# Optimization experiments

Hardware: AMD Instinct MI355X
Metric: run time of the kernel (lower is better)

## Reference

```python
import jax, jax.numpy as jnp
import numpy as np

B, N, C = 4, 4096, 384
NH, SR = 6, 2
HD = C // NH
LN_EPS = 1e-5


def setup_inputs() -> dict:
    key = jax.random.key(0)
    ks = jax.random.split(key, 8)
    s = 0.02
    return {
        "x": jax.random.normal(ks[0], (B, N, C), dtype=jnp.float32),
        "Wq": jax.random.normal(ks[1], (C, C), dtype=jnp.float32) * s,
        "bq": jnp.zeros((C,), jnp.float32),
        "Wk": jax.random.normal(ks[2], (C, C), dtype=jnp.float32) * s,
        "bk": jnp.zeros((C,), jnp.float32),
        "Wv": jax.random.normal(ks[3], (C, C), dtype=jnp.float32) * s,
        "bv": jnp.zeros((C,), jnp.float32),
        "sr_w": jax.random.normal(ks[4], (C, 1, SR, SR), dtype=jnp.float32) * s,  # depthwise OIHW
        "sr_b": jnp.zeros((C,), jnp.float32),
        "ln_g": jnp.ones((C,), jnp.float32),
        "ln_b": jnp.zeros((C,), jnp.float32),
        "Wp": jax.random.normal(ks[5], (C, C), dtype=jnp.float32) * s,
        "bp": jnp.zeros((C,), jnp.float32),
        "H": 64,
        "W": 64,
    }


def reference(x, Wq, bq, Wk, bk, Wv, bv, sr_w, sr_b, ln_g, ln_b, Wp, bp, H, W):
    Bv, Nv, Cv = x.shape
    scale = HD ** (-0.5)

    def heads(t):  # (B, L, C) -> (B, NH, L, HD)
        return t.reshape(Bv, -1, NH, HD).transpose(0, 2, 1, 3)

    q = heads(x @ Wq.T + bq)

    # spatial reduction: depthwise strided conv on (B, C, H, W)
    x_ = x.transpose(0, 2, 1).reshape(Bv, Cv, H, W)
    x_ = jax.lax.conv_general_dilated(
        x_, sr_w, window_strides=(SR, SR), padding="VALID",
        dimension_numbers=("NCHW", "OIHW", "NCHW"), feature_group_count=Cv,
    ) + sr_b[None, :, None, None]
    x_ = x_.reshape(Bv, Cv, -1).transpose(0, 2, 1)  # (B, Nk, C)

    # LayerNorm over channels
    mu = jnp.mean(x_, axis=-1, keepdims=True)
    var = jnp.mean((x_ - mu) ** 2, axis=-1, keepdims=True)
    x_ = (x_ - mu) / jnp.sqrt(var + LN_EPS) * ln_g + ln_b

    k = heads(x_ @ Wk.T + bk)
    v = heads(x_ @ Wv.T + bv)

    attn = jnp.einsum("bhqd,bhkd->bhqk", q, k) * scale
    attn = jnp.sign(attn) * jax.nn.softmax(jnp.abs(attn), axis=-1)  # 'neg' softmax
    out = jnp.einsum("bhqk,bhkd->bhqd", attn, v)
    out = out.transpose(0, 2, 1, 3).reshape(Bv, Nv, Cv)
    return out @ Wp.T + bp
```

## Files before the change

kernel.cpp:

```cpp
#include <hip/hip_runtime.h>
#include <hip/hip_bf16.h>
#include <math.h>

#define BB 4
#define NN 4096
#define CC 384
#define NHH 6
#define HDD 64
#define NKK 1024
#define LN_EPS 1e-5f

typedef _Float16 half8 __attribute__((ext_vector_type(8)));
typedef _Float16 half4v __attribute__((ext_vector_type(4)));
typedef _Float16 half2v __attribute__((ext_vector_type(2)));
typedef float f32x4 __attribute__((ext_vector_type(4)));

#define MFMA16(a, b, c) __builtin_amdgcn_mfma_f32_16x16x32_f16((a), (b), (c), 0, 0, 0)

#define GLL16(src, dst)                                                       \
    __builtin_amdgcn_global_load_lds(                                         \
        (const __attribute__((address_space(1))) void*)(src),                 \
        (__attribute__((address_space(3))) void*)(dst), 16, 0, 0)

template<int AIN, int WIN, int OUT>
__global__ __launch_bounds__(256) void gemm_mf(
    const void* __restrict__ A0, const void* __restrict__ A1,
    const _Float16* __restrict__ Whi, const _Float16* __restrict__ Wlo,
    const float* __restrict__ bias, _Float16* __restrict__ Yhi,
    _Float16* __restrict__ Ylo, float* __restrict__ Yf, float scale)
{
    constexpr bool SPLIT = (AIN != 2);
    __shared__ _Float16 AhiS[128 * 64];
    __shared__ _Float16 AloS[SPLIT ? 128 * 64 : 64];
    __shared__ _Float16 WhiS[64 * 64];
    __shared__ _Float16 WloS[(WIN == 1) ? 64 * 64 : 64];

    const int tid = threadIdx.x;
    const int bm = blockIdx.x * 128;
    const int bn = blockIdx.y * 64;
    const int w = tid >> 6, lane = tid & 63;
    const int g = lane >> 4, n15 = lane & 15;

    f32x4 zero4 = {0.f, 0.f, 0.f, 0.f};
    f32x4 acc_hi[2][4], acc_lo[SPLIT ? 2 : 1][SPLIT ? 4 : 1];
#pragma unroll
    for (int mf = 0; mf < 2; ++mf)
#pragma unroll
        for (int nt = 0; nt < 4; ++nt) {
            acc_hi[mf][nt] = zero4;
            if (SPLIT) acc_lo[mf][nt] = zero4;
        }

    for (int k0 = 0; k0 < CC; k0 += 64) {
        __syncthreads();
        if (AIN == 0) {
            const float* A = (const float*)A0;
#pragma unroll
            for (int i = 0; i < 8; ++i) {
                int id = tid + 256 * i;
                int row = id >> 4, c4 = (id & 15) * 4;
                float4 av = *reinterpret_cast<const float4*>(A + (size_t)(bm + row) * CC + k0 + c4);
                int el = row * 64 + (((c4 >> 3) ^ (row & 7)) * 8) + (c4 & 7);
                float vv[4] = {av.x, av.y, av.z, av.w};
                half4v hi, lo;
#pragma unroll
                for (int e = 0; e < 4; ++e) {
                    _Float16 h = (_Float16)vv[e];
                    hi[e] = h;
                    lo[e] = (_Float16)((vv[e] - (float)h) * 256.0f);
                }
                *reinterpret_cast<half4v*>(&AhiS[el]) = hi;
                *reinterpret_cast<half4v*>(&AloS[el]) = lo;
            }
        } else {
            const _Float16* A = (const _Float16*)A0;
#pragma unroll
            for (int i = 0; i < 4; ++i) {
                int id = tid + 256 * i;
                int row = id >> 3, dg = id & 7;
                half8 av = *reinterpret_cast<const half8*>(A + (size_t)(bm + row) * CC + k0 + dg * 8);
                int el = row * 64 + ((dg ^ (row & 7)) * 8);
                *reinterpret_cast<half8*>(&AhiS[el]) = av;
            }
        }
#pragma unroll
        for (int i = 0; i < 2; ++i) {
            int id = tid + 256 * i;
            int row = id >> 3, dg = id & 7;
            size_t go = (size_t)(bn + row) * CC + k0 + dg * 8;
            half8 wh = *reinterpret_cast<const half8*>(Whi + go);
            int el = row * 64 + ((dg ^ (row & 7)) * 8);
            *reinterpret_cast<half8*>(&WhiS[el]) = wh;
            if (WIN == 1) {
                half8 wl = *reinterpret_cast<const half8*>(Wlo + go);
                *reinterpret_cast<half8*>(&WloS[el]) = wl;
            }
        }
        __syncthreads();
#pragma unroll
        for (int kc = 0; kc < 2; ++kc) {
            const int blk = kc * 4 + g;
            half8 a_hi[2], a_lo[2], b_hi[4], b_lo[4];
#pragma unroll
            for (int mf = 0; mf < 2; ++mf) {
                int row = w * 32 + mf * 16 + n15;
                int el = row * 64 + ((blk ^ (row & 7)) * 8);
                a_hi[mf] = *reinterpret_cast<const half8*>(&AhiS[el]);
                if (SPLIT) a_lo[mf] = *reinterpret_cast<const half8*>(&AloS[el]);
            }
#pragma unroll
            for (int nt = 0; nt < 4; ++nt) {
                int row = nt * 16 + n15;
                int el = row * 64 + ((blk ^ (row & 7)) * 8);
                b_hi[nt] = *reinterpret_cast<const half8*>(&WhiS[el]);
                if (WIN == 1) b_lo[nt] = *reinterpret_cast<const half8*>(&WloS[el]);
            }
#pragma unroll
            for (int mf = 0; mf < 2; ++mf)
#pragma unroll
                for (int nt = 0; nt < 4; ++nt) {
                    acc_hi[mf][nt] = MFMA16(a_hi[mf], b_hi[nt], acc_hi[mf][nt]);
                    if (SPLIT) {
                        acc_lo[mf][nt] = MFMA16(a_hi[mf], b_lo[nt], acc_lo[mf][nt]);
                        acc_lo[mf][nt] = MFMA16(a_lo[mf], b_hi[nt], acc_lo[mf][nt]);
                    }
                }
        }
    }
#pragma unroll
    for (int nt = 0; nt < 4; ++nt) {
        int col = bn + nt * 16 + n15;
        float bc = bias[col];
#pragma unroll
        for (int mf = 0; mf < 2; ++mf)
#pragma unroll
            for (int r = 0; r < 4; ++r) {
                size_t row = bm + w * 32 + mf * 16 + g * 4 + r;
                float y = acc_hi[mf][nt][r];
                if (SPLIT) y += acc_lo[mf][nt][r] * (1.0f / 256.0f);
                y = (y + bc) * scale;
                if (OUT == 0) {
                    _Float16 h = (_Float16)y;
                    Yhi[row * CC + col] = h;
                    Ylo[row * CC + col] = (_Float16)((y - (float)h) * 256.0f);
                } else {
                    Yf[row * CC + col] = y;
                }
            }
    }
}

__global__ __launch_bounds__(256) void gemm_kv(
    const _Float16* __restrict__ Ah, const _Float16* __restrict__ Al,
    const _Float16* __restrict__ Wkh, const _Float16* __restrict__ Wkl,
    const _Float16* __restrict__ Wvh, const _Float16* __restrict__ Wvl,
    const float* __restrict__ bk, const float* __restrict__ bv,
    _Float16* __restrict__ Khi, _Float16* __restrict__ Klo,
    _Float16* __restrict__ Vt)
{
    __shared__ _Float16 AhiS[128 * 64];
    __shared__ _Float16 AloS[128 * 64];
    __shared__ _Float16 WhiS[64 * 64];
    __shared__ _Float16 WloS[64 * 64];

    const int tid = threadIdx.x;
    const int bm = blockIdx.x * 128;
    const int bn = blockIdx.y * 64;
    const int isV = blockIdx.z;
    const _Float16* Whi = isV ? Wvh : Wkh;
    const _Float16* Wlo = isV ? Wvl : Wkl;
    const float* bias = isV ? bv : bk;
    const int w = tid >> 6, lane = tid & 63;
    const int g = lane >> 4, n15 = lane & 15;

    f32x4 zero4 = {0.f, 0.f, 0.f, 0.f};
    f32x4 acc_hi[2][4], acc_lo[2][4];
#pragma unroll
    for (int mf = 0; mf < 2; ++mf)
#pragma unroll
        for (int nt = 0; nt < 4; ++nt) { acc_hi[mf][nt] = zero4; acc_lo[mf][nt] = zero4; }

    for (int k0 = 0; k0 < CC; k0 += 64) {
        __syncthreads();
#pragma unroll
        for (int i = 0; i < 4; ++i) {
            int id = tid + 256 * i;
            int row = id >> 3, dg = id & 7;
            size_t go = (size_t)(bm + row) * CC + k0 + dg * 8;
            half8 hv = *reinterpret_cast<const half8*>(Ah + go);
            half8 lv = *reinterpret_cast<const half8*>(Al + go);
            int el = row * 64 + ((dg ^ (row & 7)) * 8);
            *reinterpret_cast<half8*>(&AhiS[el]) = hv;
            *reinterpret_cast<half8*>(&AloS[el]) = lv;
        }
#pragma unroll
        for (int i = 0; i < 2; ++i) {
            int id = tid + 256 * i;
            int row = id >> 3, dg = id & 7;
            size_t go = (size_t)(bn + row) * CC + k0 + dg * 8;
            half8 wh = *reinterpret_cast<const half8*>(Whi + go);
            half8 wl = *reinterpret_cast<const half8*>(Wlo + go);
            int el = row * 64 + ((dg ^ (row & 7)) * 8);
            *reinterpret_cast<half8*>(&WhiS[el]) = wh;
            *reinterpret_cast<half8*>(&WloS[el]) = wl;
        }
        __syncthreads();
#pragma unroll
        for (int kc = 0; kc < 2; ++kc) {
            const int blk = kc * 4 + g;
            half8 a_hi[2], a_lo[2], b_hi[4], b_lo[4];
#pragma unroll
            for (int mf = 0; mf < 2; ++mf) {
                int row = w * 32 + mf * 16 + n15;
                int el = row * 64 + ((blk ^ (row & 7)) * 8);
                a_hi[mf] = *reinterpret_cast<const half8*>(&AhiS[el]);
                a_lo[mf] = *reinterpret_cast<const half8*>(&AloS[el]);
            }
#pragma unroll
            for (int nt = 0; nt < 4; ++nt) {
                int row = nt * 16 + n15;
                int el = row * 64 + ((blk ^ (row & 7)) * 8);
                b_hi[nt] = *reinterpret_cast<const half8*>(&WhiS[el]);
                b_lo[nt] = *reinterpret_cast<const half8*>(&WloS[el]);
            }
#pragma unroll
            for (int mf = 0; mf < 2; ++mf)
#pragma unroll
                for (int nt = 0; nt < 4; ++nt) {
                    acc_hi[mf][nt] = MFMA16(a_hi[mf], b_hi[nt], acc_hi[mf][nt]);
                    acc_lo[mf][nt] = MFMA16(a_hi[mf], b_lo[nt], acc_lo[mf][nt]);
                    acc_lo[mf][nt] = MFMA16(a_lo[mf], b_hi[nt], acc_lo[mf][nt]);
                }
        }
    }
#pragma unroll
    for (int nt = 0; nt < 4; ++nt) {
        int col = bn + nt * 16 + n15;
        float bc = bias[col];
#pragma unroll
        for (int mf = 0; mf < 2; ++mf)
#pragma unroll
            for (int r = 0; r < 4; ++r) {
                size_t row = bm + w * 32 + mf * 16 + g * 4 + r;
                float y = acc_hi[mf][nt][r] + acc_lo[mf][nt][r] * (1.0f / 256.0f) + bc;
                if (!isV) {
                    _Float16 h = (_Float16)y;
                    Khi[row * CC + col] = h;
                    Klo[row * CC + col] = (_Float16)((y - (float)h) * 256.0f);
                } else {
                    Vt[((row >> 10) * CC + col) * NKK + (row & 1023)] = (_Float16)y;
                }
            }
    }
}

__global__ __launch_bounds__(128)
void srconv_splitw(const float* __restrict__ x, const float* __restrict__ srw,
                   const float* __restrict__ srb, const float* __restrict__ g,
                   const float* __restrict__ beta,
                   _Float16* __restrict__ xrh, _Float16* __restrict__ xrl,
                   const float* __restrict__ Wq, const float* __restrict__ Wk,
                   const float* __restrict__ Wv, const float* __restrict__ Wp,
                   _Float16* __restrict__ wqh, _Float16* __restrict__ wql,
                   _Float16* __restrict__ wkh, _Float16* __restrict__ wkl,
                   _Float16* __restrict__ wvh, _Float16* __restrict__ wvl,
                   _Float16* __restrict__ wph) {
    const int bid = blockIdx.x;
    const int tid = threadIdx.x;
    if (bid >= BB * NKK) {
        int i = (bid - BB * NKK) * 128 + tid;
        float q = Wq[i], k = Wk[i], v = Wv[i], p = Wp[i];
        _Float16 h;
        h = (_Float16)q; wqh[i] = h; wql[i] = (_Float16)((q - (float)h) * 256.0f);
        h = (_Float16)k; wkh[i] = h; wkl[i] = (_Float16)((k - (float)h) * 256.0f);
        h = (_Float16)v; wvh[i] = h; wvl[i] = (_Float16)((v - (float)h) * 256.0f);
        wph[i] = (_Float16)p;
        return;
    }
    const int row = bid;
    const int b  = row >> 10;
    const int nk = row & 1023;
    const int oy = nk >> 5;
    const int ox = nk & 31;
    const int n0 = (2 * oy) * 64 + 2 * ox;
    const float* xb = x + ((size_t)b * NN + n0) * CC;

    float vals[3];
    float lsum = 0.f, lsum2 = 0.f;
#pragma unroll
    for (int i = 0; i < 3; ++i) {
        const int c = tid + i * 128;
        const float4 w = *reinterpret_cast<const float4*>(srw + (size_t)c * 4);
        float v = xb[c] * w.x + xb[CC + c] * w.y +
                  xb[(size_t)64 * CC + c] * w.z + xb[(size_t)65 * CC + c] * w.w + srb[c];
        vals[i] = v;
        lsum += v;
        lsum2 += v * v;
    }
#pragma unroll
    for (int off = 32; off; off >>= 1) {
        lsum  += __shfl_down(lsum, off);
        lsum2 += __shfl_down(lsum2, off);
    }
    __shared__ float ssum[2], ssum2[2];
    if ((tid & 63) == 0) { ssum[tid >> 6] = lsum; ssum2[tid >> 6] = lsum2; }
    __syncthreads();
    const float tot  = ssum[0] + ssum[1];
    const float tot2 = ssum2[0] + ssum2[1];
    const float mu  = tot * (1.0f / 384.0f);
    const float var = tot2 * (1.0f / 384.0f) - mu * mu;
    const float rstd = 1.0f / sqrtf(var + LN_EPS);

    _Float16* oh = xrh + (size_t)row * CC;
    _Float16* ol = xrl + (size_t)row * CC;
#pragma unroll
    for (int i = 0; i < 3; ++i) {
        const int c = tid + i * 128;
        float v = (vals[i] - mu) * rstd * g[c] + beta[c];
        _Float16 h = (_Float16)v;
        oh[c] = h;
        ol[c] = (_Float16)((v - (float)h) * 256.0f);
    }
}

__global__ __launch_bounds__(256, 3)
void attn_mfma(const _Float16* __restrict__ Qhi, const _Float16* __restrict__ Qlo,
               const _Float16* __restrict__ Khi, const _Float16* __restrict__ Klo,
               const _Float16* __restrict__ Vt, _Float16* __restrict__ O)
{
    __shared__ _Float16 KhiS[2][32 * 64];
    __shared__ _Float16 KloS[2][32 * 64];
    __shared__ _Float16 VTS[2][64 * 32];
    __shared__ _Float16 PWS[4][1024];

    const int tid = threadIdx.x;
    const int w = tid >> 6, lane = tid & 63;
    const int g = lane >> 4, q15 = lane & 15;
    _Float16* PW = PWS[w];

    const int qt = blockIdx.x, h = blockIdx.y, b = blockIdx.z;

    half8 qh[2][2], ql[2][2];
    {
        size_t qoff = ((size_t)b * NN + qt * 128 + w * 32 + q15) * CC + h * 64 + g * 8;
#pragma unroll
        for (int f = 0; f < 2; ++f) {
            qh[f][0] = *reinterpret_cast<const half8*>(Qhi + qoff + f * 16 * CC);
            qh[f][1] = *reinterpret_cast<const half8*>(Qhi + qoff + f * 16 * CC + 32);
            ql[f][0] = *reinterpret_cast<const half8*>(Qlo + qoff + f * 16 * CC);
            ql[f][1] = *reinterpret_cast<const half8*>(Qlo + qoff + f * 16 * CC + 32);
        }
    }
    asm volatile("s_waitcnt vmcnt(0)" ::: "memory");

    const int krow = tid >> 3, kdg = tid & 7;
    const int kscol = (kdg ^ (krow & 7)) * 8;
    const _Float16* ksrc = Khi + ((size_t)b * NKK + krow) * CC + h * 64 + kscol;
    const _Float16* lsrc = Klo + ((size_t)b * NKK + krow) * CC + h * 64 + kscol;
    const int vd = tid >> 2, vkb = tid & 3;
    const _Float16* vsrc = Vt + ((size_t)b * CC + h * 64 + vd) * NKK + ((vkb ^ ((vd >> 1) & 3)) * 8);

    f32x4 zero4 = {0.f, 0.f, 0.f, 0.f};
    f32x4 o[2][4];
#pragma unroll
    for (int f = 0; f < 2; ++f)
#pragma unroll
        for (int nt = 0; nt < 4; ++nt) o[f][nt] = zero4;
    float l[2] = {0.f, 0.f};

#define ISSUE(kt, buf)                                                        \
    {                                                                         \
        GLL16(ksrc + (size_t)(kt) * 32 * CC, &KhiS[buf][tid * 8]);            \
        GLL16(lsrc + (size_t)(kt) * 32 * CC, &KloS[buf][tid * 8]);            \
        GLL16(vsrc + (kt) * 32,              &VTS[buf][tid * 8]);             \
    }

    auto COMPUTE = [&](const _Float16* KH, const _Float16* KL, const _Float16* VT) {
        float ls[2] = {0.f, 0.f};
#pragma unroll
        for (int mt = 0; mt < 2; ++mt) {
            f32x4 sh[2], sl[2];
#pragma unroll
            for (int f = 0; f < 2; ++f) { sh[f] = zero4; sl[f] = zero4; }
            __builtin_amdgcn_s_setprio(1);
#pragma unroll
            for (int kc = 0; kc < 2; ++kc) {
                int key = mt * 16 + q15;
                int el = key * 64 + (((kc * 4 + g) ^ (key & 7)) * 8);
                half8 ah = *reinterpret_cast<const half8*>(&KH[el]);
                half8 al = *reinterpret_cast<const half8*>(&KL[el]);
#pragma unroll
                for (int f = 0; f < 2; ++f) {
                    sh[f] = MFMA16(ah, qh[f][kc], sh[f]);
                    sl[f] = MFMA16(ah, ql[f][kc], sl[f]);
                    sl[f] = MFMA16(al, qh[f][kc], sl[f]);
                }
            }
            __builtin_amdgcn_s_setprio(0);
            int elw = q15 * 32 + (((mt * 2 + (g >> 1)) ^ ((q15 >> 1) & 3)) * 8) + (g & 1) * 4;
#pragma unroll
            for (int f = 0; f < 2; ++f) {
                half4v pk;
#pragma unroll
                for (int r = 0; r < 4; ++r) {
                    float sv = sh[f][r] + sl[f][r] * (1.0f / 256.0f);
                    float e = __expf(fabsf(sv));
                    ls[f] += e;
                    pk[r] = (_Float16)__builtin_copysignf(e, sv);
                }
                *reinterpret_cast<half4v*>(&PW[elw + f * 512]) = pk;
            }
        }
#pragma unroll
        for (int f = 0; f < 2; ++f) {
            ls[f] += __shfl_xor(ls[f], 16);
            ls[f] += __shfl_xor(ls[f], 32);
            l[f] += ls[f];
        }

        __builtin_amdgcn_s_setprio(1);
        {
            int pel = q15 * 32 + ((g ^ ((q15 >> 1) & 3)) * 8);
            half8 pa0 = *reinterpret_cast<const half8*>(&PW[pel]);
            half8 pa1 = *reinterpret_cast<const half8*>(&PW[pel + 512]);
#pragma unroll
            for (int nt = 0; nt < 4; ++nt) {
                int d = nt * 16 + q15;
                int vel = d * 32 + ((g ^ ((d >> 1) & 3)) * 8);
                half8 vb = *reinterpret_cast<const half8*>(&VT[vel]);
                o[0][nt] = MFMA16(pa0, vb, o[0][nt]);
                o[1][nt] = MFMA16(pa1, vb, o[1][nt]);
            }
        }
        __builtin_amdgcn_s_setprio(0);
    };

    ISSUE(0, 0);

#pragma unroll 1
    for (int kt2 = 0; kt2 < 32; kt2 += 2) {
        ISSUE(kt2 + 1, 1);
        asm volatile("s_waitcnt vmcnt(3)" ::: "memory");
        __builtin_amdgcn_s_barrier();
        COMPUTE(KhiS[0], KloS[0], VTS[0]);
        asm volatile("" ::: "memory");
        __builtin_amdgcn_s_barrier();

        if (kt2 + 2 < 32) {
            ISSUE(kt2 + 2, 0);
            asm volatile("s_waitcnt vmcnt(3)" ::: "memory");
        } else {
            asm volatile("s_waitcnt vmcnt(0)" ::: "memory");
        }
        __builtin_amdgcn_s_barrier();
        COMPUTE(KhiS[1], KloS[1], VTS[1]);
        asm volatile("" ::: "memory");
        __builtin_amdgcn_s_barrier();
    }
#undef ISSUE

#pragma unroll
    for (int f = 0; f < 2; ++f) {
        float rl = 1.0f / l[f];
        float rlq[4];
#pragma unroll
        for (int r = 0; r < 4; ++r) rlq[r] = __shfl(rl, g * 4 + r);
#pragma unroll
        for (int nt = 0; nt < 4; ++nt)
#pragma unroll
            for (int r = 0; r < 4; ++r) {
                size_t row = (size_t)b * NN + qt * 128 + w * 32 + f * 16 + g * 4 + r;
                O[row * CC + h * 64 + nt * 16 + q15] = (_Float16)(o[f][nt][r] * rlq[r]);
            }
    }
}

extern "C" void kernel_launch(void* const* d_in, const int* in_sizes, int n_in,
                              void* d_out, int out_size, void* d_ws, size_t ws_size,
                              hipStream_t stream) {
    const float* x   = (const float*)d_in[0];
    const float* Wq  = (const float*)d_in[1];
    const float* bq  = (const float*)d_in[2];
    const float* Wk  = (const float*)d_in[3];
    const float* bk  = (const float*)d_in[4];
    const float* Wv  = (const float*)d_in[5];
    const float* bv  = (const float*)d_in[6];
    const float* srw = (const float*)d_in[7];
    const float* srb = (const float*)d_in[8];
    const float* lng = (const float*)d_in[9];
    const float* lnb = (const float*)d_in[10];
    const float* Wp  = (const float*)d_in[11];
    const float* bp  = (const float*)d_in[12];
    float* out = (float*)d_out;

    char* wsb = (char*)d_ws;
    _Float16* Qhi  = (_Float16*)wsb;
    _Float16* Qlo  = (_Float16*)(wsb + 12582912);
    _Float16* XRhi = (_Float16*)(wsb + 25165824);
    _Float16* XRlo = (_Float16*)(wsb + 28311552);
    _Float16* Khi  = (_Float16*)(wsb + 31457280);
    _Float16* Klo  = (_Float16*)(wsb + 34603008);
    _Float16* Vt   = (_Float16*)(wsb + 37748736);
    _Float16* Wqh  = (_Float16*)(wsb + 40894464);
    _Float16* Wql  = Wqh + 147456;
    _Float16* Wkh  = Wql + 147456;
    _Float16* Wkl  = Wkh + 147456;
    _Float16* Wvh  = Wkl + 147456;
    _Float16* Wvl  = Wvh + 147456;
    _Float16* Wph  = Wvl + 147456;
    _Float16* Ob   = Qlo;

    srconv_splitw<<<dim3(BB * NKK + 1152), dim3(128), 0, stream>>>(
        x, srw, srb, lng, lnb, XRhi, XRlo,
        Wq, Wk, Wv, Wp, Wqh, Wql, Wkh, Wkl, Wvh, Wvl, Wph);
    gemm_mf<0, 1, 0><<<dim3(128, 6), 256, 0, stream>>>(
        x, nullptr, Wqh, Wql, bq, Qhi, Qlo, nullptr, 0.125f);
    gemm_kv<<<dim3(32, 6, 2), 256, 0, stream>>>(
        XRhi, XRlo, Wkh, Wkl, Wvh, Wvl, bk, bv, Khi, Klo, Vt);
    attn_mfma<<<dim3(32, 6, 4), 256, 0, stream>>>(Qhi, Qlo, Khi, Klo, Vt, Ob);
    gemm_mf<2, 2, 2><<<dim3(128, 6), 256, 0, stream>>>(
        Ob, nullptr, Wph, nullptr, bp, nullptr, nullptr, out, 1.0f);
}
```

Before: 129.4 us.

## Merge Q/K/V projections into one launch and triple-buffer attention K/V tiles

Merges the Q projection and the K/V projection kernels into a single kernel whose blocks choose their mode from the block index, cutting one launch and letting the small K/V work fill gaps left by the Q work. The attention kernel moves from double to triple buffering of K/V tiles, so each prefetch is issued right after a compute step instead of behind a second barrier. The cross-lane row-sum reduction is also deferred to the end of the attention kernel. The output GEMM is split into its own specialised kernel. Triple buffering uses more LDS per block, which may reduce occupancy.

```diff
diff --git a/kernel.cpp b/kernel.cpp
--- a/kernel.cpp
+++ b/kernel.cpp
@@ -22,18 +22,12 @@
         (const __attribute__((address_space(1))) void*)(src),                 \
         (__attribute__((address_space(3))) void*)(dst), 16, 0, 0)
 
-template<int AIN, int WIN, int OUT>
-__global__ __launch_bounds__(256) void gemm_mf(
-    const void* __restrict__ A0, const void* __restrict__ A1,
-    const _Float16* __restrict__ Whi, const _Float16* __restrict__ Wlo,
-    const float* __restrict__ bias, _Float16* __restrict__ Yhi,
-    _Float16* __restrict__ Ylo, float* __restrict__ Yf, float scale)
+__global__ __launch_bounds__(256) void gemm_out(
+    const _Float16* __restrict__ A, const _Float16* __restrict__ Whi,
+    const float* __restrict__ bias, float* __restrict__ Yf)
 {
-    constexpr bool SPLIT = (AIN != 2);
     __shared__ _Float16 AhiS[128 * 64];
-    __shared__ _Float16 AloS[SPLIT ? 128 * 64 : 64];
     __shared__ _Float16 WhiS[64 * 64];
-    __shared__ _Float16 WloS[(WIN == 1) ? 64 * 64 : 64];
 
     const int tid = threadIdx.x;
     const int bm = blockIdx.x * 128;
@@ -42,24 +36,116 @@
     const int g = lane >> 4, n15 = lane & 15;
 
     f32x4 zero4 = {0.f, 0.f, 0.f, 0.f};
-    f32x4 acc_hi[2][4], acc_lo[SPLIT ? 2 : 1][SPLIT ? 4 : 1];
+    f32x4 acc[2][4];
 #pragma unroll
     for (int mf = 0; mf < 2; ++mf)
 #pragma unroll
-        for (int nt = 0; nt < 4; ++nt) {
-            acc_hi[mf][nt] = zero4;
-            if (SPLIT) acc_lo[mf][nt] = zero4;
-        }
+        for (int nt = 0; nt < 4; ++nt) acc[mf][nt] = zero4;
 
     for (int k0 = 0; k0 < CC; k0 += 64) {
         __syncthreads();
-        if (AIN == 0) {
-            const float* A = (const float*)A0;
+#pragma unroll
+        for (int i = 0; i < 4; ++i) {
+            int id = tid + 256 * i;
+            int row = id >> 3, dg = id & 7;
+            half8 av = *reinterpret_cast<const half8*>(A + (size_t)(bm + row) * CC + k0 + dg * 8);
+            int el = row * 64 + ((dg ^ (row & 7)) * 8);
+            *reinterpret_cast<half8*>(&AhiS[el]) = av;
+        }
+#pragma unroll
+        for (int i = 0; i < 2; ++i) {
+            int id = tid + 256 * i;
+            int row = id >> 3, dg = id & 7;
+            half8 wh = *reinterpret_cast<const half8*>(Whi + (size_t)(bn + row) * CC + k0 + dg * 8);
+            int el = row * 64 + ((dg ^ (row & 7)) * 8);
+            *reinterpret_cast<half8*>(&WhiS[el]) = wh;
+        }
+        __syncthreads();
+#pragma unroll
+        for (int kc = 0; kc < 2; ++kc) {
+            const int blk = kc * 4 + g;
+            half8 a_hi[2], b_hi[4];
+#pragma unroll
+            for (int mf = 0; mf < 2; ++mf) {
+                int row = w * 32 + mf * 16 + n15;
+                a_hi[mf] = *reinterpret_cast<const half8*>(&AhiS[row * 64 + ((blk ^ (row & 7)) * 8)]);
+            }
+#pragma unroll
+            for (int nt = 0; nt < 4; ++nt) {
+                int row = nt * 16 + n15;
+                b_hi[nt] = *reinterpret_cast<const half8*>(&WhiS[row * 64 + ((blk ^ (row & 7)) * 8)]);
+            }
+#pragma unroll
+            for (int mf = 0; mf < 2; ++mf)
+#pragma unroll
+                for (int nt = 0; nt < 4; ++nt)
+                    acc[mf][nt] = MFMA16(a_hi[mf], b_hi[nt], acc[mf][nt]);
+        }
+    }
+#pragma unroll
+    for (int nt = 0; nt < 4; ++nt) {
+        int col = bn + nt * 16 + n15;
+        float bc = bias[col];
+#pragma unroll
+        for (int mf = 0; mf < 2; ++mf)
+#pragma unroll
+            for (int r = 0; r < 4; ++r) {
+                size_t row = bm + w * 32 + mf * 16 + g * 4 + r;
+                Yf[row * CC + col] = acc[mf][nt][r] + bc;
+            }
+    }
+}
+
+__global__ __launch_bounds__(256) void proj_all(
+    const float* __restrict__ x,
+    const _Float16* __restrict__ XRh, const _Float16* __restrict__ XRl,
+    const _Float16* __restrict__ Wqh, const _Float16* __restrict__ Wql,
+    const _Float16* __restrict__ Wkh, const _Float16* __restrict__ Wkl,
+    const _Float16* __restrict__ Wvh, const _Float16* __restrict__ Wvl,
+    const float* __restrict__ bq, const float* __restrict__ bk,
+    const float* __restrict__ bv,
+    _Float16* __restrict__ Qhi, _Float16* __restrict__ Qlo,
+    _Float16* __restrict__ Khi, _Float16* __restrict__ Klo,
+    _Float16* __restrict__ Vt)
+{
+    __shared__ _Float16 AhiS[128 * 64];
+    __shared__ _Float16 AloS[128 * 64];
+    __shared__ _Float16 WhiS[64 * 64];
+    __shared__ _Float16 WloS[64 * 64];
+
+    const int bid = blockIdx.x;
+    const int tid = threadIdx.x;
+    int bm, bn, mode;
+    if (bid < 768) {
+        bm = (bid & 127) * 128; bn = (bid >> 7) * 64; mode = 0;
+    } else {
+        int idx = bid - 768;
+        bm = (idx & 31) * 128; bn = ((idx >> 5) % 6) * 64;
+        mode = (idx >= 192) ? 2 : 1;
+    }
+    const _Float16* Whi = (mode == 0) ? Wqh : ((mode == 1) ? Wkh : Wvh);
+    const _Float16* Wlo = (mode == 0) ? Wql : ((mode == 1) ? Wkl : Wvl);
+    const float* bias   = (mode == 0) ? bq  : ((mode == 1) ? bk  : bv);
+    const float scale   = (mode == 0) ? 0.125f : 1.0f;
+
+    const int w = tid >> 6, lane = tid & 63;
+    const int g = lane >> 4, n15 = lane & 15;
+
+    f32x4 zero4 = {0.f, 0.f, 0.f, 0.f};
+    f32x4 acc_hi[2][4], acc_lo[2][4];
+#pragma unroll
+    for (int mf = 0; mf < 2; ++mf)
+#pragma unroll
+        for (int nt = 0; nt < 4; ++nt) { acc_hi[mf][nt] = zero4; acc_lo[mf][nt] = zero4; }
+
+    for (int k0 = 0; k0 < CC; k0 += 64) {
+        __syncthreads();
+        if (mode == 0) {
 #pragma unroll
             for (int i = 0; i < 8; ++i) {
                 int id = tid + 256 * i;
                 int row = id >> 4, c4 = (id & 15) * 4;
-                float4 av = *reinterpret_cast<const float4*>(A + (size_t)(bm + row) * CC + k0 + c4);
+                float4 av = *reinterpret_cast<const float4*>(x + (size_t)(bm + row) * CC + k0 + c4);
                 int el = row * 64 + (((c4 >> 3) ^ (row & 7)) * 8) + (c4 & 7);
                 float vv[4] = {av.x, av.y, av.z, av.w};
                 half4v hi, lo;
@@ -73,125 +159,17 @@
                 *reinterpret_cast<half4v*>(&AloS[el]) = lo;
             }
         } else {
-            const _Float16* A = (const _Float16*)A0;
 #pragma unroll
             for (int i = 0; i < 4; ++i) {
                 int id = tid + 256 * i;
                 int row = id >> 3, dg = id & 7;
-                half8 av = *reinterpret_cast<const half8*>(A + (size_t)(bm + row) * CC + k0 + dg * 8);
+                size_t go = (size_t)(bm + row) * CC + k0 + dg * 8;
+                half8 hv = *reinterpret_cast<const half8*>(XRh + go);
+                half8 lv = *reinterpret_cast<const half8*>(XRl + go);
                 int el = row * 64 + ((dg ^ (row & 7)) * 8);
-                *reinterpret_cast<half8*>(&AhiS[el]) = av;
-            }
-        }
-#pragma unroll
-        for (int i = 0; i < 2; ++i) {
-            int id = tid + 256 * i;
-            int row = id >> 3, dg = id & 7;
-            size_t go = (size_t)(bn + row) * CC + k0 + dg * 8;
-            half8 wh = *reinterpret_cast<const half8*>(Whi + go);
-            int el = row * 64 + ((dg ^ (row & 7)) * 8);
-            *reinterpret_cast<half8*>(&WhiS[el]) = wh;
-            if (WIN == 1) {
-                half8 wl = *reinterpret_cast<const half8*>(Wlo + go);
-                *reinterpret_cast<half8*>(&WloS[el]) = wl;
-            }
-        }
-        __syncthreads();
-#pragma unroll
-        for (int kc = 0; kc < 2; ++kc) {
-            const int blk = kc * 4 + g;
-            half8 a_hi[2], a_lo[2], b_hi[4], b_lo[4];
-#pragma unroll
-            for (int mf = 0; mf < 2; ++mf) {
-                int row = w * 32 + mf * 16 + n15;
-                int el = row * 64 + ((blk ^ (row & 7)) * 8);
-                a_hi[mf] = *reinterpret_cast<const half8*>(&AhiS[el]);
-                if (SPLIT) a_lo[mf] = *reinterpret_cast<const half8*>(&AloS[el]);
-            }
-#pragma unroll
-            for (int nt = 0; nt < 4; ++nt) {
-                int row = nt * 16 + n15;
-                int el = row * 64 + ((blk ^ (row & 7)) * 8);
-                b_hi[nt] = *reinterpret_cast<const half8*>(&WhiS[el]);
-                if (WIN == 1) b_lo[nt] = *reinterpret_cast<const half8*>(&WloS[el]);
-            }
-#pragma unroll
-            for (int mf = 0; mf < 2; ++mf)
-#pragma unroll
-                for (int nt = 0; nt < 4; ++nt) {
-                    acc_hi[mf][nt] = MFMA16(a_hi[mf], b_hi[nt], acc_hi[mf][nt]);
-                    if (SPLIT) {
-                        acc_lo[mf][nt] = MFMA16(a_hi[mf], b_lo[nt], acc_lo[mf][nt]);
-                        acc_lo[mf][nt] = MFMA16(a_lo[mf], b_hi[nt], acc_lo[mf][nt]);
-                    }
-                }
-        }
-    }
-#pragma unroll
-    for (int nt = 0; nt < 4; ++nt) {
-        int col = bn + nt * 16 + n15;
-        float bc = bias[col];
-#pragma unroll
-        for (int mf = 0; mf < 2; ++mf)
-#pragma unroll
-            for (int r = 0; r < 4; ++r) {
-                size_t row = bm + w * 32 + mf * 16 + g * 4 + r;
-                float y = acc_hi[mf][nt][r];
-                if (SPLIT) y += acc_lo[mf][nt][r] * (1.0f / 256.0f);
-                y = (y + bc) * scale;
-                if (OUT == 0) {
-                    _Float16 h = (_Float16)y;
-                    Yhi[row * CC + col] = h;
-                    Ylo[row * CC + col] = (_Float16)((y - (float)h) * 256.0f);
-                } else {
-                    Yf[row * CC + col] = y;
-                }
-            }
-    }
-}
-
-__global__ __launch_bounds__(256) void gemm_kv(
-    const _Float16* __restrict__ Ah, const _Float16* __restrict__ Al,
-    const _Float16* __restrict__ Wkh, const _Float16* __restrict__ Wkl,
-    const _Float16* __restrict__ Wvh, const _Float16* __restrict__ Wvl,
-    const float* __restrict__ bk, const float* __restrict__ bv,
-    _Float16* __restrict__ Khi, _Float16* __restrict__ Klo,
-    _Float16* __restrict__ Vt)
-{
-    __shared__ _Float16 AhiS[128 * 64];
-    __shared__ _Float16 AloS[128 * 64];
-    __shared__ _Float16 WhiS[64 * 64];
-    __shared__ _Float16 WloS[64 * 64];
-
-    const int tid = threadIdx.x;
-    const int bm = blockIdx.x * 128;
-    const int bn = blockIdx.y * 64;
-    const int isV = blockIdx.z;
-    const _Float16* Whi = isV ? Wvh : Wkh;
-    const _Float16* Wlo = isV ? Wvl : Wkl;
-    const float* bias = isV ? bv : bk;
-    const int w = tid >> 6, lane = tid & 63;
-    const int g = lane >> 4, n15 = lane & 15;
-
-    f32x4 zero4 = {0.f, 0.f, 0.f, 0.f};
-    f32x4 acc_hi[2][4], acc_lo[2][4];
-#pragma unroll
-    for (int mf = 0; mf < 2; ++mf)
-#pragma unroll
-        for (int nt = 0; nt < 4; ++nt) { acc_hi[mf][nt] = zero4; acc_lo[mf][nt] = zero4; }
-
-    for (int k0 = 0; k0 < CC; k0 += 64) {
-        __syncthreads();
-#pragma unroll
-        for (int i = 0; i < 4; ++i) {
-            int id = tid + 256 * i;
-            int row = id >> 3, dg = id & 7;
-            size_t go = (size_t)(bm + row) * CC + k0 + dg * 8;
-            half8 hv = *reinterpret_cast<const half8*>(Ah + go);
-            half8 lv = *reinterpret_cast<const half8*>(Al + go);
-            int el = row * 64 + ((dg ^ (row & 7)) * 8);
-            *reinterpret_cast<half8*>(&AhiS[el]) = hv;
-            *reinterpret_cast<half8*>(&AloS[el]) = lv;
+                *reinterpret_cast<half8*>(&AhiS[el]) = hv;
+                *reinterpret_cast<half8*>(&AloS[el]) = lv;
+            }
         }
 #pragma unroll
         for (int i = 0; i < 2; ++i) {
@@ -242,8 +220,12 @@
 #pragma unroll
             for (int r = 0; r < 4; ++r) {
                 size_t row = bm + w * 32 + mf * 16 + g * 4 + r;
-                float y = acc_hi[mf][nt][r] + acc_lo[mf][nt][r] * (1.0f / 256.0f) + bc;
-                if (!isV) {
+                float y = (acc_hi[mf][nt][r] + acc_lo[mf][nt][r] * (1.0f / 256.0f) + bc) * scale;
+                if (mode == 0) {
+                    _Float16 h = (_Float16)y;
+                    Qhi[row * CC + col] = h;
+                    Qlo[row * CC + col] = (_Float16)((y - (float)h) * 256.0f);
+                } else if (mode == 1) {
                     _Float16 h = (_Float16)y;
                     Khi[row * CC + col] = h;
                     Klo[row * CC + col] = (_Float16)((y - (float)h) * 256.0f);
@@ -328,9 +310,9 @@
                const _Float16* __restrict__ Khi, const _Float16* __restrict__ Klo,
                const _Float16* __restrict__ Vt, _Float16* __restrict__ O)
 {
-    __shared__ _Float16 KhiS[2][32 * 64];
-    __shared__ _Float16 KloS[2][32 * 64];
-    __shared__ _Float16 VTS[2][64 * 32];
+    __shared__ _Float16 KhiS[3][32 * 64];
+    __shared__ _Float16 KloS[3][32 * 64];
+    __shared__ _Float16 VTS[3][64 * 32];
     __shared__ _Float16 PWS[4][1024];
 
     const int tid = threadIdx.x;
@@ -376,7 +358,6 @@
     }
 
     auto COMPUTE = [&](const _Float16* KH, const _Float16* KL, const _Float16* VT) {
-        float ls[2] = {0.f, 0.f};
 #pragma unroll
         for (int mt = 0; mt < 2; ++mt) {
             f32x4 sh[2], sl[2];
@@ -405,17 +386,11 @@
                 for (int r = 0; r < 4; ++r) {
                     float sv = sh[f][r] + sl[f][r] * (1.0f / 256.0f);
                     float e = __expf(fabsf(sv));
-                    ls[f] += e;
+                    l[f] += e;
                     pk[r] = (_Float16)__builtin_copysignf(e, sv);
                 }
                 *reinterpret_cast<half4v*>(&PW[elw + f * 512]) = pk;
             }
-        }
-#pragma unroll
-        for (int f = 0; f < 2; ++f) {
-            ls[f] += __shfl_xor(ls[f], 16);
-            ls[f] += __shfl_xor(ls[f], 32);
-            l[f] += ls[f];
         }
 
         __builtin_amdgcn_s_setprio(1);
@@ -436,29 +411,38 @@
     };
 
     ISSUE(0, 0);
+    ISSUE(1, 1);
 
 #pragma unroll 1
-    for (int kt2 = 0; kt2 < 32; kt2 += 2) {
-        ISSUE(kt2 + 1, 1);
+    for (int base = 0; base < 30; base += 3) {
         asm volatile("s_waitcnt vmcnt(3)" ::: "memory");
         __builtin_amdgcn_s_barrier();
         COMPUTE(KhiS[0], KloS[0], VTS[0]);
-        asm volatile("" ::: "memory");
-        __builtin_amdgcn_s_barrier();
-
-        if (kt2 + 2 < 32) {
-            ISSUE(kt2 + 2, 0);
-            asm volatile("s_waitcnt vmcnt(3)" ::: "memory");
-        } else {
-            asm volatile("s_waitcnt vmcnt(0)" ::: "memory");
-        }
+        ISSUE(base + 2, 2);
+
+        asm volatile("s_waitcnt vmcnt(3)" ::: "memory");
         __builtin_amdgcn_s_barrier();
         COMPUTE(KhiS[1], KloS[1], VTS[1]);
-        asm volatile("" ::: "memory");
+        ISSUE(base + 3, 0);
+
+        asm volatile("s_waitcnt vmcnt(3)" ::: "memory");
         __builtin_amdgcn_s_barrier();
-    }
+        COMPUTE(KhiS[2], KloS[2], VTS[2]);
+        if (base + 4 < 32) ISSUE(base + 4, 1);
+    }
+    asm volatile("s_waitcnt vmcnt(3)" ::: "memory");
+    __builtin_amdgcn_s_barrier();
+    COMPUTE(KhiS[0], KloS[0], VTS[0]);
+    asm volatile("s_waitcnt vmcnt(0)" ::: "memory");
+    __builtin_amdgcn_s_barrier();
+    COMPUTE(KhiS[1], KloS[1], VTS[1]);
 #undef ISSUE
 
+#pragma unroll
+    for (int f = 0; f < 2; ++f) {
+        l[f] += __shfl_xor(l[f], 16);
+        l[f] += __shfl_xor(l[f], 32);
+    }
 #pragma unroll
     for (int f = 0; f < 2; ++f) {
         float rl = 1.0f / l[f];
@@ -513,11 +497,9 @@
     srconv_splitw<<<dim3(BB * NKK + 1152), dim3(128), 0, stream>>>(
         x, srw, srb, lng, lnb, XRhi, XRlo,
         Wq, Wk, Wv, Wp, Wqh, Wql, Wkh, Wkl, Wvh, Wvl, Wph);
-    gemm_mf<0, 1, 0><<<dim3(128, 6), 256, 0, stream>>>(
-        x, nullptr, Wqh, Wql, bq, Qhi, Qlo, nullptr, 0.125f);
-    gemm_kv<<<dim3(32, 6, 2), 256, 0, stream>>>(
-        XRhi, XRlo, Wkh, Wkl, Wvh, Wvl, bk, bv, Khi, Klo, Vt);
+    proj_all<<<dim3(1152), 256, 0, stream>>>(
+        x, XRhi, XRlo, Wqh, Wql, Wkh, Wkl, Wvh, Wvl,
+        bq, bk, bv, Qhi, Qlo, Khi, Klo, Vt);
     attn_mfma<<<dim3(32, 6, 4), 256, 0, stream>>>(Qhi, Qlo, Khi, Klo, Vt, Ob);
-    gemm_mf<2, 2, 2><<<dim3(128, 6), 256, 0, stream>>>(
-        Ob, nullptr, Wph, nullptr, bp, nullptr, nullptr, out, 1.0f);
+    gemm_out<<<dim3(128, 6), 256, 0, stream>>>(Ob, Wph, bp, out);
 }
```

Measured after the change: 125.2 us. -3.2%, faster.
